# Kernel tuning notes

Hardware: AMD Instinct MI355X
Metric: run time of the kernel (lower is better)

The kernel has to match this reference:

```python
import jax, jax.numpy as jnp
import numpy as np

NUM_HEADS = 32
NUM_KV = 8
HEAD_DIM = 128


def rotate_half(x):
    half = x.shape[-1] // 2
    x1, x2 = x[..., :half], x[..., half:]
    return jnp.concatenate([-x2, x1], axis=-1)


def apply_rope(x, cos, sin):
    # x: [B, H, S, D]; cos/sin: [S, D] broadcast over batch and heads
    return x * cos + rotate_half(x) * sin


def setup_inputs() -> dict:
    key = jax.random.key(0)
    kx, kqkv, kout = jax.random.split(key, 3)
    B, S, H = 2, 2048, 4096
    x = jax.random.normal(kx, (B, S, H), dtype=jnp.float32)
    Wqkv = jax.random.normal(kqkv, (H, NUM_HEADS * HEAD_DIM + 2 * NUM_KV * HEAD_DIM), dtype=jnp.float32) * (H ** -0.5)
    Wout = jax.random.normal(kout, (H, H), dtype=jnp.float32) * (H ** -0.5)
    # realistic RoPE tables (seq, head_dim)
    inv_freq = 1.0 / (10000.0 ** (np.arange(0, HEAD_DIM, 2, dtype=np.float32) / HEAD_DIM))
    freqs = np.outer(np.arange(S, dtype=np.float32), inv_freq)  # [S, D/2]
    emb = np.concatenate([freqs, freqs], axis=-1)  # [S, D]
    cos = jnp.asarray(np.cos(emb), dtype=jnp.float32)
    sin = jnp.asarray(np.sin(emb), dtype=jnp.float32)
    return {"x": x, "cos": cos, "sin": sin, "Wqkv": Wqkv, "Wout": Wout}


def reference(x, cos, sin, Wqkv, Wout):
    B, S, H = x.shape
    nh, nkv, hd = NUM_HEADS, NUM_KV, HEAD_DIM
    qkv = x @ Wqkv  # [B, S, (nh+2*nkv)*hd]
    q, k, v = jnp.split(qkv, [nh * hd, nh * hd + nkv * hd], axis=-1)
    q = q.reshape(B, S, nh, hd).transpose(0, 2, 1, 3)   # [B, nh, S, hd]
    k = k.reshape(B, S, nkv, hd).transpose(0, 2, 1, 3)  # [B, nkv, S, hd]
    v = v.reshape(B, S, nkv, hd).transpose(0, 2, 1, 3)
    q = apply_rope(q, cos, sin)
    k = apply_rope(k, cos, sin)
    group = nh // nkv
    k = jnp.repeat(k, group, axis=1)  # repeat_interleave over head dim
    v = jnp.repeat(v, group, axis=1)
    scale = 1.0 / jnp.sqrt(jnp.asarray(hd, dtype=x.dtype))
    scores = jnp.einsum('bhqd,bhkd->bhqk', q, k) * scale  # [B, nh, S, S]
    causal = jnp.triu(jnp.ones((S, S), dtype=bool), k=1)
    scores = jnp.where(causal, -jnp.inf, scores)
    w = jax.nn.softmax(scores, axis=-1)
    out = jnp.einsum('bhqk,bhkd->bhqd', w, v)  # [B, nh, S, hd]
    out = out.transpose(0, 2, 1, 3).reshape(B, S, nh * hd)
    return out @ Wout
```

## Files before the change

### kernel.cpp

```cpp
#include <hip/hip_runtime.h>

typedef unsigned short u16;
typedef __attribute__((ext_vector_type(8))) short s16x8;
typedef __attribute__((ext_vector_type(4))) short s16x4;
typedef __attribute__((ext_vector_type(4))) float f32x4;

#define DEVI __device__ __forceinline__

DEVI u16 f2b(float f) {
  union { float f; unsigned u; } v; v.f = f;
  unsigned r = v.u + 0x7FFFu + ((v.u >> 16) & 1u);
  return (u16)(r >> 16);
}
DEVI float b2f(u16 h) {
  union { unsigned u; float f; } v; v.u = ((unsigned)h) << 16;
  return v.f;
}

typedef const __attribute__((address_space(1))) void gas_void;
typedef __attribute__((address_space(3))) void las_void;
DEVI void gload16(const void* g, void* l) {
  __builtin_amdgcn_global_load_lds((gas_void*)g, (las_void*)l, 16, 0, 0);
}

__global__ void prep_kernel(const float* __restrict__ x, const float* __restrict__ W,
                            u16* __restrict__ xb, u16* __restrict__ Wt) {
  __shared__ __attribute__((aligned(16))) u16 tile[64][68];
  const int t = threadIdx.x;
  const int bid = blockIdx.x;
  if (bid < 6144) {
    const int n0 = (bid % 96) * 64, k0 = (bid / 96) * 64;
    const int N = 6144, K = 4096;
#pragma unroll
    for (int i = 0; i < 4; ++i) {
      int c = i * 256 + t;
      int r = c >> 4, q = c & 15;
      float4 v = *(const float4*)(W + (size_t)(k0 + r) * N + n0 + q * 4);
      s16x4 o = {(short)f2b(v.x), (short)f2b(v.y), (short)f2b(v.z), (short)f2b(v.w)};
      *(s16x4*)&tile[r][q * 4] = o;
    }
    __syncthreads();
#pragma unroll
    for (int i = 0; i < 2; ++i) {
      int c = i * 256 + t;
      int n_ = c >> 3, ck = (c & 7) * 8;
      s16x8 o;
#pragma unroll
      for (int j = 0; j < 8; ++j) o[j] = (short)tile[ck + j][n_];
      *(s16x8*)(Wt + (size_t)(n0 + n_) * K + k0 + ck) = o;
    }
  } else {
    int i = (bid - 6144) * 256 + t;
    const float* p = x + (size_t)i * 8;
    float4 u = *(const float4*)p;
    float4 v = *(const float4*)(p + 4);
    s16x8 o = {(short)f2b(u.x), (short)f2b(u.y), (short)f2b(u.z), (short)f2b(u.w),
               (short)f2b(v.x), (short)f2b(v.y), (short)f2b(v.z), (short)f2b(v.w)};
    *(s16x8*)(xb + (size_t)i * 8) = o;
  }
}

__global__ void trans_bf16(const float* __restrict__ W, u16* __restrict__ Wt, int K, int N) {
  __shared__ __attribute__((aligned(16))) u16 tile[64][68];
  const int t = threadIdx.x;
  const int n0 = blockIdx.x * 64, k0 = blockIdx.y * 64;
#pragma unroll
  for (int i = 0; i < 4; ++i) {
    int c = i * 256 + t;
    int r = c >> 4, q = c & 15;
    float4 v = *(const float4*)(W + (size_t)(k0 + r) * N + n0 + q * 4);
    s16x4 o = {(short)f2b(v.x), (short)f2b(v.y), (short)f2b(v.z), (short)f2b(v.w)};
    *(s16x4*)&tile[r][q * 4] = o;
  }
  __syncthreads();
#pragma unroll
  for (int i = 0; i < 2; ++i) {
    int c = i * 256 + t;
    int n_ = c >> 3, ck = (c & 7) * 8;
    s16x8 o;
#pragma unroll
    for (int j = 0; j < 8; ++j) o[j] = (short)tile[ck + j][n_];
    *(s16x8*)(Wt + (size_t)(n0 + n_) * K + k0 + ck) = o;
  }
}

__global__ __launch_bounds__(512, 2) void gemm128_g1(const u16* __restrict__ A,
                                                     const u16* __restrict__ Bt,
                                                     u16* __restrict__ C, int M, int N, int K) {
  __shared__ __attribute__((aligned(16))) u16 As[2][128 * 64];
  __shared__ __attribute__((aligned(16))) u16 Bs[2][256 * 64];
  const int t = threadIdx.x;
  const int nbn = N >> 8;
  const int nwg = (M >> 7) * nbn;
  const int chunk = nwg >> 3;
  const int id = (blockIdx.x & 7) * chunk + (blockIdx.x >> 3);
  const int row0 = (id / nbn) << 7, col0 = (id % nbn) << 8;
  const int w = t >> 6, lane = t & 63, lc = lane & 15, lg = lane >> 4;
  const int wm = (w >> 2) * 64;
  const int wn4 = (w & 3);
  const int sw7 = lc & 7;

  const f32x4 FZ = {0.f, 0.f, 0.f, 0.f};
  f32x4 acc[4][4];
#pragma unroll
  for (int i = 0; i < 4; ++i)
#pragma unroll
    for (int j = 0; j < 4; ++j) acc[i][j] = FZ;

  const int ra = t >> 3;
  const int sa = (t & 7) ^ (ra & 7);
  const int bg0 = ((ra >> 5) << 6) | (ra & 31);

#define G1_STG_A(kt, sl)                                                          \
  {                                                                               \
    const u16* ap = A + (size_t)(row0 + ra) * K + ((kt) << 6) + (sa << 3);        \
    gload16(ap, (u16*)As[sl] + t * 8);                                            \
    gload16(ap + (size_t)64 * K, (u16*)As[sl] + (512 + t) * 8);                   \
  }
#define G1_STG_B(kt, H, sl)                                                       \
  {                                                                               \
    const u16* bp = Bt + (size_t)(col0 + bg0 + ((H) << 5)) * K + ((kt) << 6) + (sa << 3); \
    gload16(bp, (u16*)Bs[sl] + (H)*8192 + t * 8);                                 \
    gload16(bp + (size_t)128 * K, (u16*)Bs[sl] + (H)*8192 + (512 + t) * 8);       \
  }
#define G1_LOAD_A(buf)                                                            \
  _Pragma("unroll") for (int mf = 0; mf < 4; ++mf)                                \
  _Pragma("unroll") for (int ks = 0; ks < 2; ++ks)                                \
    af[mf][ks] = *(const s16x8*)(As[buf] + (wm + mf * 16 + lc) * 64 +             \
                                 (((ks * 4 + lg) ^ sw7) << 3));
#define G1_LOAD_B(NH, buf)                                                        \
  _Pragma("unroll") for (int nfl = 0; nfl < 2; ++nfl)                             \
  _Pragma("unroll") for (int ks = 0; ks < 2; ++ks)                                \
    bfv[nfl][ks] = *(const s16x8*)(Bs[buf] + ((NH)*128 + wn4 * 32 + nfl * 16 + lc) * 64 + \
                                   (((ks * 4 + lg) ^ sw7) << 3));
#define G1_MFMA(NH)                                                               \
  _Pragma("unroll") for (int ks = 0; ks < 2; ++ks)                                \
  _Pragma("unroll") for (int mf = 0; mf < 4; ++mf)                                \
  _Pragma("unroll") for (int nfl = 0; nfl < 2; ++nfl)                             \
    acc[mf][(NH)*2 + nfl] = __builtin_amdgcn_mfma_f32_16x16x32_bf16(              \
        af[mf][ks], bfv[nfl][ks], acc[mf][(NH)*2 + nfl], 0, 0, 0);
#define BAR __builtin_amdgcn_s_barrier()
#define PRIO1 __builtin_amdgcn_s_setprio(1)
#define PRIO0 __builtin_amdgcn_s_setprio(0)

  s16x8 af[4][2], bfv[2][2];
  const int NT = K >> 6, TM = NT - 1;

  G1_STG_A(0, 0) G1_STG_B(0, 0, 0) G1_STG_B(0, 1, 0)
  asm volatile("s_waitcnt vmcnt(2)" ::: "memory");
  BAR;

  for (int kt = 0; kt < NT; ++kt) {
    const int buf = kt & 1, nb = buf ^ 1;
    const int tp1 = (kt + 1) & TM;
    G1_LOAD_A(buf)
    G1_LOAD_B(0, buf)
    G1_STG_A(tp1, nb)
    G1_STG_B(tp1, 0, nb)
    BAR; PRIO1; G1_MFMA(0) PRIO0;
    asm volatile("s_waitcnt vmcnt(4)" ::: "memory");
    BAR;
    G1_LOAD_B(1, buf)
    G1_STG_B(tp1, 1, nb)
    BAR; PRIO1; G1_MFMA(1) PRIO0;
    asm volatile("s_waitcnt vmcnt(2)" ::: "memory");
    BAR;
  }
  asm volatile("s_waitcnt vmcnt(0)" ::: "memory");
#undef G1_STG_A
#undef G1_STG_B
#undef G1_LOAD_A
#undef G1_LOAD_B
#undef G1_MFMA
#undef BAR
#undef PRIO1
#undef PRIO0

#pragma unroll
  for (int mf = 0; mf < 4; ++mf)
#pragma unroll
    for (int nf = 0; nf < 4; ++nf)
#pragma unroll
      for (int r = 0; r < 4; ++r) {
        const int rg = row0 + wm + mf * 16 + lg * 4 + r;
        const int cg = col0 + wn4 * 64 + (nf >> 1) * 32 + (nf & 1) * 16 + lc;
        C[(size_t)rg * N + cg] = f2b(acc[mf][nf][r]);
      }
}

__global__ __launch_bounds__(512, 2) void gemm256_g2(const u16* __restrict__ A,
                                                     const u16* __restrict__ Bt,
                                                     float* __restrict__ C, int M, int N, int K) {
  __shared__ __attribute__((aligned(16))) u16 As[2][2][128 * 64];
  __shared__ __attribute__((aligned(16))) u16 Bs[2][2][128 * 64];
  const int t = threadIdx.x;
  const int nbn = N >> 8;
  const int nwg = (M >> 8) * nbn;
  const int chunk = nwg >> 3;
  const int id = (blockIdx.x & 7) * chunk + (blockIdx.x >> 3);
  const int row0 = (id / nbn) << 8, col0 = (id % nbn) << 8;
  const int w = t >> 6, lane = t & 63, lc = lane & 15, lg = lane >> 4;
  const int wqm = (w >> 2) * 64;
  const int wqn = (w & 3) * 32;
  const int sw7 = lc & 7;

  const f32x4 FZ = {0.f, 0.f, 0.f, 0.f};
  f32x4 acc[4][4][2];
#pragma unroll
  for (int q = 0; q < 4; ++q)
#pragma unroll
    for (int i = 0; i < 4; ++i)
#pragma unroll
      for (int j = 0; j < 2; ++j) acc[q][i][j] = FZ;

  const int s_r0 = t >> 3, s_r1 = (512 + t) >> 3;
  const int s_s = t & 7;

#define STG_A(kt, H, sl)                                                                   \
  {                                                                                        \
    gload16(A + (size_t)(row0 + (H)*128 + s_r0) * K + ((kt) << 6) + ((s_s ^ (s_r0 & 7)) << 3), \
            (u16*)As[sl][H] + t * 8);                                                      \
    gload16(A + (size_t)(row0 + (H)*128 + s_r1) * K + ((kt) << 6) + ((s_s ^ (s_r1 & 7)) << 3), \
            (u16*)As[sl][H] + (512 + t) * 8);                                              \
  }
#define STG_B(kt, H, sl)                                                                   \
  {                                                                                        \
    gload16(Bt + (size_t)(col0 + (H)*128 + s_r0) * K + ((kt) << 6) + ((s_s ^ (s_r0 & 7)) << 3), \
            (u16*)Bs[sl][H] + t * 8);                                                      \
    gload16(Bt + (size_t)(col0 + (H)*128 + s_r1) * K + ((kt) << 6) + ((s_s ^ (s_r1 & 7)) << 3), \
            (u16*)Bs[sl][H] + (512 + t) * 8);                                              \
  }
#define LOAD_A(MH, buf)                                                           \
  _Pragma("unroll") for (int mf = 0; mf < 4; ++mf)                                \
  _Pragma("unroll") for (int ks = 0; ks < 2; ++ks)                                \
    af[mf][ks] = *(const s16x8*)(As[buf][MH] + (wqm + mf * 16 + lc) * 64 +        \
                                 (((ks * 4 + lg) ^ sw7) << 3));
#define LOAD_B(NH, buf, DST)                                                      \
  _Pragma("unroll") for (int nf = 0; nf < 2; ++nf)                                \
  _Pragma("unroll") for (int ks = 0; ks < 2; ++ks)                                \
    DST[nf][ks] = *(const s16x8*)(Bs[buf][NH] + (wqn + nf * 16 + lc) * 64 +       \
                                  (((ks * 4 + lg) ^ sw7) << 3));
#define MFMA_Q(q, BV)                                                             \
  _Pragma("unroll") for (int ks = 0; ks < 2; ++ks)                                \
  _Pragma("unroll") for (int mf = 0; mf < 4; ++mf)                                \
  _Pragma("unroll") for (int nf = 0; nf < 2; ++nf)                                \
    acc[q][mf][nf] = __builtin_amdgcn_mfma_f32_16x16x32_bf16(                     \
        af[mf][ks], BV[nf][ks], acc[q][mf][nf], 0, 0, 0);
#define BAR __builtin_amdgcn_s_barrier()
#define PRIO1 __builtin_amdgcn_s_setprio(1)
#define PRIO0 __builtin_amdgcn_s_setprio(0)
#define WAIT6 asm volatile("s_waitcnt vmcnt(6)" ::: "memory")

  s16x8 af[4][2], bfv0[2][2], bfv1[2][2];
  const int NT = K >> 6, TM = NT - 1;

  STG_A(0, 0, 0) STG_B(0, 0, 0) STG_B(0, 1, 0) STG_A(0, 1, 0)
  STG_A(1, 0, 1) STG_B(1, 0, 1) STG_B(1, 1, 1)
  WAIT6;
  BAR;

  for (int kt = 0; kt < NT; ++kt) {
    const int buf = kt & 1, nb = buf ^ 1;
    const int tp1 = (kt + 1) & TM, tp2 = (kt + 2) & TM;
    LOAD_A(0, buf) LOAD_B(0, buf, bfv0)
    STG_A(tp1, 1, nb)
    BAR; PRIO1; MFMA_Q(0, bfv0) PRIO0; BAR;
    LOAD_B(1, buf, bfv1)
    STG_A(tp2, 0, buf)
    BAR; PRIO1; MFMA_Q(1, bfv1) PRIO0; BAR;
    LOAD_A(1, buf)
    STG_B(tp2, 0, buf)
    BAR; PRIO1; MFMA_Q(2, bfv1) PRIO0; BAR;
    STG_B(tp2, 1, buf)
    BAR; PRIO1; MFMA_Q(3, bfv0) PRIO0;
    WAIT6;
    BAR;
  }
  asm volatile("s_waitcnt vmcnt(0)" ::: "memory");
  BAR;
#undef STG_A
#undef STG_B
#undef LOAD_A
#undef LOAD_B
#undef MFMA_Q
#undef BAR
#undef PRIO1
#undef PRIO0
#undef WAIT6

  const int qmh[4] = {0, 0, 1, 1}, qnh[4] = {0, 1, 1, 0};
#pragma unroll
  for (int q = 0; q < 4; ++q)
#pragma unroll
    for (int mf = 0; mf < 4; ++mf)
#pragma unroll
      for (int nf = 0; nf < 2; ++nf)
#pragma unroll
        for (int r = 0; r < 4; ++r) {
          const int rg = row0 + qmh[q] * 128 + wqm + mf * 16 + lg * 4 + r;
          const int cg = col0 + qnh[q] * 128 + wqn + nf * 16 + lc;
          C[(size_t)rg * N + cg] = acc[q][mf][nf][r];
        }
}

__global__ void rope_kernel(u16* __restrict__ qkv, const float* __restrict__ cosb,
                            const float* __restrict__ sinb) {
  const int bs = blockIdx.x;
  const int s = bs & 2047;
  u16* row = qkv + (size_t)bs * 6144;
  const float* cr = cosb + s * 128;
  const float* sr = sinb + s * 128;
  const float SC2 = 0.08838834764831845f * 1.44269504088896340736f;
  for (int p = threadIdx.x; p < 320; p += 256) {
    int head = p >> 3, dc = (p & 7) * 8;
    int ci = head * 128 + dc;
    const float m = (head < 32) ? SC2 : 1.0f;
    s16x8 a = *(const s16x8*)&row[ci];
    s16x8 bb = *(const s16x8*)&row[ci + 64];
    float4 c0 = *(const float4*)(cr + dc), c1 = *(const float4*)(cr + dc + 4);
    float4 s0 = *(const float4*)(sr + dc), s1 = *(const float4*)(sr + dc + 4);
    float cv[8] = {c0.x, c0.y, c0.z, c0.w, c1.x, c1.y, c1.z, c1.w};
    float sv[8] = {s0.x, s0.y, s0.z, s0.w, s1.x, s1.y, s1.z, s1.w};
    s16x8 o1, o2;
#pragma unroll
    for (int j = 0; j < 8; ++j) {
      float x1 = b2f((u16)a[j]), x2 = b2f((u16)bb[j]);
      o1[j] = (short)f2b((x1 * cv[j] - x2 * sv[j]) * m);
      o2[j] = (short)f2b((x2 * cv[j] + x1 * sv[j]) * m);
    }
    *(s16x8*)&row[ci] = o1;
    *(s16x8*)&row[ci + 64] = o2;
  }
}

__global__ void vtrans_kernel(const u16* __restrict__ qkv, u16* __restrict__ v_t) {
  __shared__ __attribute__((aligned(16))) u16 tile[64][72];
  const int t = threadIdx.x;
  const int s0 = blockIdx.x * 64;
  const int d0 = blockIdx.y * 64;
  const int bk = blockIdx.z;
  const int b = bk >> 3, kvh = bk & 7;
  const int slot = t & 7, r0 = t >> 3;
#pragma unroll
  for (int i = 0; i < 2; ++i) {
    int s_ = r0 + 32 * i;
    *(s16x8*)&tile[s_][slot * 8] =
        *(const s16x8*)(qkv + (size_t)(b * 2048 + s0 + s_) * 6144 + 5120 + kvh * 128 + d0 + slot * 8);
  }
  __syncthreads();
#pragma unroll
  for (int i = 0; i < 2; ++i) {
    int d_ = r0 + 32 * i;
    s16x8 v;
#pragma unroll
    for (int j = 0; j < 8; ++j) v[j] = (short)tile[slot * 8 + j][d_];
    *(s16x8*)(v_t + ((size_t)bk * 128 + d0 + d_) * 2048 + s0 + slot * 8) = v;
  }
}

__global__ void __launch_bounds__(256, 2) attn_kernel(const u16* __restrict__ qkv,
                                                      const u16* __restrict__ v_t,
                                                      u16* __restrict__ attn) {
  __shared__ __attribute__((aligned(16))) u16 Ks[64][136];
  __shared__ __attribute__((aligned(16))) u16 Vs[128][72];
  __shared__ __attribute__((aligned(16))) u16 Ps[4][32][72];
  const int t = threadIdx.x;
  const int f = blockIdx.x;
  const int xcd = f & 7, ix = f >> 3;
  const int g = (xcd << 1) | (ix >> 6);
  const int r_ = ix & 63;
  const int b = g >> 3, kvh = g & 7;
  const int qt = 15 - (r_ >> 2);
  const int h = kvh * 4 + (r_ & 3);
  const int q0 = qt * 128;
  const int w = t >> 6, lane = t & 63, lc = lane & 15, lg = lane >> 4;
  const int qw = q0 + w * 32;

  const u16* qbase = qkv + (size_t)(b * 2048) * 6144 + h * 128;
  const u16* kbase = qkv + (size_t)(b * 2048) * 6144 + 4096 + kvh * 128;
  const u16* vbase = v_t + (size_t)(b * 8 + kvh) * 128 * 2048;

  s16x8 qf[2][4];
#pragma unroll
  for (int mf = 0; mf < 2; ++mf)
#pragma unroll
    for (int ks = 0; ks < 4; ++ks)
      qf[mf][ks] = *(const s16x8*)(qbase + (size_t)(qw + mf * 16 + lc) * 6144 + ks * 32 + lg * 8);

  const f32x4 FZ = {0.f, 0.f, 0.f, 0.f};
  f32x4 o_acc[2][8];
  float m_run[2][4], l_run[2][4];
#pragma unroll
  for (int mf = 0; mf < 2; ++mf) {
#pragma unroll
    for (int nf = 0; nf < 8; ++nf) o_acc[mf][nf] = FZ;
#pragma unroll
    for (int r = 0; r < 4; ++r) { m_run[mf][r] = -3e38f; l_run[mf][r] = 0.f; }
  }

  const int ntiles = q0 / 64 + 2;
  s16x8 kr[4], vr[4];
#pragma unroll
  for (int i = 0; i < 4; ++i) {
    int c = i * 256 + t;
    kr[i] = *(const s16x8*)(kbase + (size_t)(c >> 4) * 6144 + (c & 15) * 8);
    vr[i] = *(const s16x8*)(vbase + (size_t)(c >> 3) * 2048 + (c & 7) * 8);
  }

  for (int kt = 0; kt < ntiles; ++kt) {
    const int k0 = kt * 64;
    __syncthreads();
#pragma unroll
    for (int i = 0; i < 4; ++i) {
      int c = i * 256 + t;
      *(s16x8*)&Ks[c >> 4][(c & 15) * 8] = kr[i];
      *(s16x8*)&Vs[c >> 3][(c & 7) * 8] = vr[i];
    }
    __syncthreads();
    if (kt + 1 < ntiles) {
      int k1 = k0 + 64;
#pragma unroll
      for (int i = 0; i < 4; ++i) {
        int c = i * 256 + t;
        kr[i] = *(const s16x8*)(kbase + (size_t)(k1 + (c >> 4)) * 6144 + (c & 15) * 8);
        vr[i] = *(const s16x8*)(vbase + (size_t)(c >> 3) * 2048 + k1 + (c & 7) * 8);
      }
    }
    if (k0 > qw + 31) continue;

    f32x4 sacc[2][4];
#pragma unroll
    for (int mf = 0; mf < 2; ++mf)
#pragma unroll
      for (int nf = 0; nf < 4; ++nf) sacc[mf][nf] = FZ;
#pragma unroll
    for (int ks = 0; ks < 4; ++ks) {
      s16x8 kf[4];
#pragma unroll
      for (int nf = 0; nf < 4; ++nf)
        kf[nf] = *(const s16x8*)&Ks[nf * 16 + lc][ks * 32 + lg * 8];
#pragma unroll
      for (int mf = 0; mf < 2; ++mf)
#pragma unroll
        for (int nf = 0; nf < 4; ++nf)
          sacc[mf][nf] = __builtin_amdgcn_mfma_f32_16x16x32_bf16(qf[mf][ks], kf[nf], sacc[mf][nf], 0, 0, 0);
    }

#pragma unroll
    for (int mf = 0; mf < 2; ++mf) {
      float pm[4] = {-3e38f, -3e38f, -3e38f, -3e38f};
      const bool dm = (k0 + 63 > qw + mf * 16);
      if (dm) {
#pragma unroll
        for (int nf = 0; nf < 4; ++nf) {
          int kv = k0 + nf * 16 + lc;
#pragma unroll
          for (int r = 0; r < 4; ++r) {
            int qg = qw + mf * 16 + lg * 4 + r;
            float sv = (kv <= qg) ? sacc[mf][nf][r] : -3e38f;
            sacc[mf][nf][r] = sv;
            pm[r] = fmaxf(pm[r], sv);
          }
        }
      } else {
#pragma unroll
        for (int nf = 0; nf < 4; ++nf)
#pragma unroll
          for (int r = 0; r < 4; ++r) pm[r] = fmaxf(pm[r], sacc[mf][nf][r]);
      }
#pragma unroll
      for (int r = 0; r < 4; ++r) {
        pm[r] = fmaxf(pm[r], __shfl_xor(pm[r], 1));
        pm[r] = fmaxf(pm[r], __shfl_xor(pm[r], 2));
        pm[r] = fmaxf(pm[r], __shfl_xor(pm[r], 4));
        pm[r] = fmaxf(pm[r], __shfl_xor(pm[r], 8));
      }
      bool need = false;
#pragma unroll
      for (int r = 0; r < 4; ++r) need |= (pm[r] > m_run[mf][r] + 8.0f);
      if (__any(need)) {
#pragma unroll
        for (int r = 0; r < 4; ++r) {
          float mnew = fmaxf(m_run[mf][r], pm[r]);
          float fsc = exp2f(m_run[mf][r] - mnew);
          m_run[mf][r] = mnew;
          l_run[mf][r] *= fsc;
#pragma unroll
          for (int nf = 0; nf < 8; ++nf) o_acc[mf][nf][r] *= fsc;
        }
      }
      float psum[4] = {0.f, 0.f, 0.f, 0.f};
#pragma unroll
      for (int nf = 0; nf < 4; ++nf)
#pragma unroll
        for (int r = 0; r < 4; ++r) {
          float p = exp2f(sacc[mf][nf][r] - m_run[mf][r]);
          psum[r] += p;
          Ps[w][mf * 16 + lg * 4 + r][nf * 16 + lc] = f2b(p);
        }
#pragma unroll
      for (int r = 0; r < 4; ++r) {
        float ps = psum[r];
        ps += __shfl_xor(ps, 1);
        ps += __shfl_xor(ps, 2);
        ps += __shfl_xor(ps, 4);
        ps += __shfl_xor(ps, 8);
        l_run[mf][r] += ps;
      }
    }
#pragma unroll
    for (int ks = 0; ks < 2; ++ks) {
      s16x8 pf[2];
#pragma unroll
      for (int mf = 0; mf < 2; ++mf)
        pf[mf] = *(const s16x8*)&Ps[w][mf * 16 + lc][ks * 32 + lg * 8];
#pragma unroll
      for (int nf = 0; nf < 8; ++nf) {
        s16x8 vf = *(const s16x8*)&Vs[nf * 16 + lc][ks * 32 + lg * 8];
#pragma unroll
        for (int mf = 0; mf < 2; ++mf)
          o_acc[mf][nf] = __builtin_amdgcn_mfma_f32_16x16x32_bf16(pf[mf], vf, o_acc[mf][nf], 0, 0, 0);
      }
    }
  }

#pragma unroll
  for (int mf = 0; mf < 2; ++mf)
#pragma unroll
    for (int r = 0; r < 4; ++r) {
      float inv = 1.0f / l_run[mf][r];
      int qg = qw + mf * 16 + lg * 4 + r;
#pragma unroll
      for (int nf = 0; nf < 8; ++nf)
        attn[(size_t)(b * 2048 + qg) * 4096 + h * 128 + nf * 16 + lc] =
            f2b(o_acc[mf][nf][r] * inv);
    }
}

extern "C" void kernel_launch(void* const* d_in, const int* in_sizes, int n_in,
                              void* d_out, int out_size, void* d_ws, size_t ws_size,
                              hipStream_t stream) {
  (void)in_sizes; (void)n_in; (void)out_size; (void)ws_size;
  const float* x = (const float*)d_in[0];
  const float* cosb = (const float*)d_in[1];
  const float* sinb = (const float*)d_in[2];
  const float* Wqkv = (const float*)d_in[3];
  const float* Wout = (const float*)d_in[4];
  float* out = (float*)d_out;
  char* ws = (char*)d_ws;

  u16* buf0 = (u16*)ws;
  u16* buf1 = (u16*)(ws + 50331648);
  u16* regc = (u16*)(ws + 100663296);

  prep_kernel<<<14336, 256, 0, stream>>>(x, Wqkv, regc, buf0);
  gemm128_g1<<<768, 512, 0, stream>>>(regc, buf0, buf1, 4096, 6144, 4096);
  rope_kernel<<<4096, 256, 0, stream>>>(buf1, cosb, sinb);
  vtrans_kernel<<<dim3(32, 2, 16), 256, 0, stream>>>(buf1, regc);
  attn_kernel<<<1024, 256, 0, stream>>>(buf1, regc, buf0);
  trans_bf16<<<dim3(64, 64), 256, 0, stream>>>(Wout, regc, 4096, 4096);
  gemm256_g2<<<256, 512, 0, stream>>>(buf0, regc, out, 4096, 4096, 4096);
}
```

Before: 545.0 us.

## Rotate three B half-tile LDS buffers in GEMM and compute softmax row sums via MFMA

The GEMM's B staging moves from two full 256-row buffers to three rotating 128-row half-tile buffers. This cuts LDS use while keeping each half-tile prefetch one slot ahead. In the attention kernel, the per-row softmax denominator is now accumulated with an extra MFMA against a ones vector over the bf16 P tile, replacing scalar summation and four xor-shuffle reductions. The row sum therefore comes from bf16-rounded P values, which matches the weights actually used for P·V but changes numerics slightly. It also adds two MFMAs per k-step.

```diff
diff --git a/kernel.cpp b/kernel.cpp
--- a/kernel.cpp
+++ b/kernel.cpp
@@ -88,7 +88,7 @@
                                                      const u16* __restrict__ Bt,
                                                      u16* __restrict__ C, int M, int N, int K) {
   __shared__ __attribute__((aligned(16))) u16 As[2][128 * 64];
-  __shared__ __attribute__((aligned(16))) u16 Bs[2][256 * 64];
+  __shared__ __attribute__((aligned(16))) u16 Bs[3][128 * 64];
   const int t = threadIdx.x;
   const int nbn = N >> 8;
   const int nwg = (M >> 7) * nbn;
@@ -117,21 +117,21 @@
     gload16(ap, (u16*)As[sl] + t * 8);                                            \
     gload16(ap + (size_t)64 * K, (u16*)As[sl] + (512 + t) * 8);                   \
   }
-#define G1_STG_B(kt, H, sl)                                                       \
+#define G1_STG_B(kt, H, BP)                                                       \
   {                                                                               \
     const u16* bp = Bt + (size_t)(col0 + bg0 + ((H) << 5)) * K + ((kt) << 6) + (sa << 3); \
-    gload16(bp, (u16*)Bs[sl] + (H)*8192 + t * 8);                                 \
-    gload16(bp + (size_t)128 * K, (u16*)Bs[sl] + (H)*8192 + (512 + t) * 8);       \
+    gload16(bp, (BP) + t * 8);                                                    \
+    gload16(bp + (size_t)128 * K, (BP) + (512 + t) * 8);                          \
   }
 #define G1_LOAD_A(buf)                                                            \
   _Pragma("unroll") for (int mf = 0; mf < 4; ++mf)                                \
   _Pragma("unroll") for (int ks = 0; ks < 2; ++ks)                                \
     af[mf][ks] = *(const s16x8*)(As[buf] + (wm + mf * 16 + lc) * 64 +             \
                                  (((ks * 4 + lg) ^ sw7) << 3));
-#define G1_LOAD_B(NH, buf)                                                        \
+#define G1_LOAD_B(BP)                                                             \
   _Pragma("unroll") for (int nfl = 0; nfl < 2; ++nfl)                             \
   _Pragma("unroll") for (int ks = 0; ks < 2; ++ks)                                \
-    bfv[nfl][ks] = *(const s16x8*)(Bs[buf] + ((NH)*128 + wn4 * 32 + nfl * 16 + lc) * 64 + \
+    bfv[nfl][ks] = *(const s16x8*)((BP) + (wn4 * 32 + nfl * 16 + lc) * 64 +       \
                                    (((ks * 4 + lg) ^ sw7) << 3));
 #define G1_MFMA(NH)                                                               \
   _Pragma("unroll") for (int ks = 0; ks < 2; ++ks)                                \
@@ -146,7 +146,11 @@
   s16x8 af[4][2], bfv[2][2];
   const int NT = K >> 6, TM = NT - 1;
 
-  G1_STG_A(0, 0) G1_STG_B(0, 0, 0) G1_STG_B(0, 1, 0)
+  u16* Ba = (u16*)Bs[0];
+  u16* Bb = (u16*)Bs[1];
+  u16* Bc = (u16*)Bs[2];
+
+  G1_STG_A(0, 0) G1_STG_B(0, 0, Ba) G1_STG_B(0, 1, Bb)
   asm volatile("s_waitcnt vmcnt(2)" ::: "memory");
   BAR;
 
@@ -154,17 +158,18 @@
     const int buf = kt & 1, nb = buf ^ 1;
     const int tp1 = (kt + 1) & TM;
     G1_LOAD_A(buf)
-    G1_LOAD_B(0, buf)
+    G1_LOAD_B(Ba)
     G1_STG_A(tp1, nb)
-    G1_STG_B(tp1, 0, nb)
+    G1_STG_B(tp1, 0, Bc)
     BAR; PRIO1; G1_MFMA(0) PRIO0;
     asm volatile("s_waitcnt vmcnt(4)" ::: "memory");
     BAR;
-    G1_LOAD_B(1, buf)
-    G1_STG_B(tp1, 1, nb)
+    G1_LOAD_B(Bb)
+    G1_STG_B(tp1, 1, Ba)
     BAR; PRIO1; G1_MFMA(1) PRIO0;
     asm volatile("s_waitcnt vmcnt(2)" ::: "memory");
     BAR;
+    u16* x_ = Ba; u16* y_ = Bb; Ba = Bc; Bb = x_; Bc = y_;
   }
   asm volatile("s_waitcnt vmcnt(0)" ::: "memory");
 #undef G1_STG_A
@@ -388,14 +393,18 @@
       qf[mf][ks] = *(const s16x8*)(qbase + (size_t)(qw + mf * 16 + lc) * 6144 + ks * 32 + lg * 8);
 
   const f32x4 FZ = {0.f, 0.f, 0.f, 0.f};
+  const short ONE = (short)0x3F80;
+  const s16x8 ONES = {ONE, ONE, ONE, ONE, ONE, ONE, ONE, ONE};
   f32x4 o_acc[2][8];
-  float m_run[2][4], l_run[2][4];
+  f32x4 l9[2];
+  float m_run[2][4];
 #pragma unroll
   for (int mf = 0; mf < 2; ++mf) {
 #pragma unroll
     for (int nf = 0; nf < 8; ++nf) o_acc[mf][nf] = FZ;
-#pragma unroll
-    for (int r = 0; r < 4; ++r) { m_run[mf][r] = -3e38f; l_run[mf][r] = 0.f; }
+    l9[mf] = FZ;
+#pragma unroll
+    for (int r = 0; r < 4; ++r) m_run[mf][r] = -3e38f;
   }
 
   const int ntiles = q0 / 64 + 2;
@@ -484,29 +493,18 @@
           float mnew = fmaxf(m_run[mf][r], pm[r]);
           float fsc = exp2f(m_run[mf][r] - mnew);
           m_run[mf][r] = mnew;
-          l_run[mf][r] *= fsc;
+          l9[mf][r] *= fsc;
 #pragma unroll
           for (int nf = 0; nf < 8; ++nf) o_acc[mf][nf][r] *= fsc;
         }
       }
-      float psum[4] = {0.f, 0.f, 0.f, 0.f};
 #pragma unroll
       for (int nf = 0; nf < 4; ++nf)
 #pragma unroll
         for (int r = 0; r < 4; ++r) {
           float p = exp2f(sacc[mf][nf][r] - m_run[mf][r]);
-          psum[r] += p;
           Ps[w][mf * 16 + lg * 4 + r][nf * 16 + lc] = f2b(p);
         }
-#pragma unroll
-      for (int r = 0; r < 4; ++r) {
-        float ps = psum[r];
-        ps += __shfl_xor(ps, 1);
-        ps += __shfl_xor(ps, 2);
-        ps += __shfl_xor(ps, 4);
-        ps += __shfl_xor(ps, 8);
-        l_run[mf][r] += ps;
-      }
     }
 #pragma unroll
     for (int ks = 0; ks < 2; ++ks) {
@@ -514,6 +512,9 @@
 #pragma unroll
       for (int mf = 0; mf < 2; ++mf)
         pf[mf] = *(const s16x8*)&Ps[w][mf * 16 + lc][ks * 32 + lg * 8];
+#pragma unroll
+      for (int mf = 0; mf < 2; ++mf)
+        l9[mf] = __builtin_amdgcn_mfma_f32_16x16x32_bf16(pf[mf], ONES, l9[mf], 0, 0, 0);
 #pragma unroll
       for (int nf = 0; nf < 8; ++nf) {
         s16x8 vf = *(const s16x8*)&Vs[nf * 16 + lc][ks * 32 + lg * 8];
@@ -528,7 +529,7 @@
   for (int mf = 0; mf < 2; ++mf)
 #pragma unroll
     for (int r = 0; r < 4; ++r) {
-      float inv = 1.0f / l_run[mf][r];
+      float inv = 1.0f / l9[mf][r];
       int qg = qw + mf * 16 + lg * 4 + r;
 #pragma unroll
       for (int nf = 0; nf < 8; ++nf)
```

New measurement: 538.0 us. No clear change (-1.3%).
